# Kernel optimization log

Hardware: AMD Instinct MI355X
Metric: run time of the kernel (lower is better)

The kernel has to match this reference:

```python
import jax, jax.numpy as jnp
import numpy as np

WINDOW = (7, 7, 7)
DIM = 192
HEADS = 6
B_ = 256
NW = 32
N = int(np.prod(WINDOW))


def _relative_position_index(window_size):
    coords = np.stack(np.meshgrid(*[np.arange(w) for w in window_size], indexing='ij'))
    cf = coords.reshape(len(window_size), -1)  # (3, N)
    rel = cf[:, :, None] - cf[:, None, :]      # (3, N, N)
    rel = rel.transpose(1, 2, 0).copy()        # (N, N, 3)
    for i, w in enumerate(window_size):
        rel[:, :, i] += w - 1
    rel[:, :, 0] *= (2 * window_size[1] - 1) * (2 * window_size[2] - 1)
    rel[:, :, 1] *= 2 * window_size[2] - 1
    return rel.sum(-1).astype(np.int32)       # (N, N)


def setup_inputs() -> dict:
    key = jax.random.key(0)
    ks = jax.random.split(key, 8)
    table_rows = int(np.prod([2 * w - 1 for w in WINDOW]))  # 2197
    s = 0.02
    return {
        'skip': jax.random.normal(ks[0], (B_, N, DIM), jnp.float32),
        'x_up': jax.random.normal(ks[1], (B_, N, DIM), jnp.float32),
        'mask': jax.random.normal(ks[2], (NW, N, N), jnp.float32),
        'rel_index': jnp.asarray(_relative_position_index(WINDOW)),
        'table': s * jax.random.normal(ks[3], (table_rows, HEADS), jnp.float32),
        'kv_w': jax.random.normal(ks[4], (DIM, 2 * DIM), jnp.float32) / np.sqrt(DIM),
        'kv_b': jnp.zeros((2 * DIM,), jnp.float32),
        'proj_w': jax.random.normal(ks[5], (DIM, DIM), jnp.float32) / np.sqrt(DIM),
        'proj_b': jnp.zeros((DIM,), jnp.float32),
    }


def reference(skip, x_up, mask, rel_index, table, kv_w, kv_b, proj_w, proj_b):
    B, n, C = skip.shape
    H = HEADS
    D = C // H
    scale = D ** -0.5
    # kv projection: (B, N, 2C) -> k, v each (B, H, N, D)
    kv = skip @ kv_w + kv_b
    kv = kv.reshape(B, n, 2, H, D)
    k = kv[:, :, 0].transpose(0, 2, 1, 3)
    v = kv[:, :, 1].transpose(0, 2, 1, 3)
    q = (x_up.reshape(B, n, H, D).transpose(0, 2, 1, 3)) * scale
    attn = jnp.einsum('bhnd,bhmd->bhnm', q, k)  # (B, H, N, N)
    # gathered relative position bias: (N, N, H) -> (H, N, N)
    bias = table[rel_index].transpose(2, 0, 1)
    attn = attn + bias[None]
    nW = mask.shape[0]
    attn = attn.reshape(B // nW, nW, H, n, n) + mask[None, :, None]
    attn = jax.nn.softmax(attn.reshape(B, H, n, n), axis=-1)
    x = jnp.einsum('bhnm,bhmd->bhnd', attn, v)
    x = x.transpose(0, 2, 1, 3).reshape(B, n, C)
    return x @ proj_w + proj_b
```

## Files before the change

kernel.cpp:

```cpp
#include <hip/hip_runtime.h>
#include <hip/hip_bf16.h>

#define B_  256
#define N_  343
#define C_  192
#define H_  6
#define D_  32
#define NW_ 32
#define NN_ (N_*N_)
#define TROWS 2197
#define NP_ 352
#define PLANE (NP_*NP_)

typedef unsigned int  uint32;
typedef unsigned short u16;
typedef __attribute__((ext_vector_type(8))) short bf16x8;
typedef __attribute__((ext_vector_type(4))) float f32x4;

union frag8 { uint4 u4; bf16x8 h8; short s[8]; };

__device__ __forceinline__ float bf2f(u16 u){
  union { uint32 u; float f; } v; v.u = ((uint32)u) << 16; return v.f;
}
__device__ __forceinline__ u16 f2bf(float f){
  union { float f; uint32 u; } v; v.f = f;
  uint32 u = v.u;
  return (u16)((u + 0x7FFFu + ((u >> 16) & 1u)) >> 16);
}

__device__ __forceinline__ bool detect_f32(const uint32* w){
  int c = 0;
  #pragma unroll
  for (int u = 0; u < 32; u++){
    int e = (w[u*37] >> 7) & 0xFF;
    c += (e > 150);
  }
  return c >= 3;
}
__device__ __forceinline__ float ldf(const void* p, size_t i, bool f32){
  return f32 ? ((const float*)p)[i] : bf2f(((const u16*)p)[i]);
}
__device__ __forceinline__ void stf(void* p, size_t i, float v, bool f32){
  if (f32) ((float*)p)[i] = v;
  else     ((u16*)p)[i]   = f2bf(v);
}

__device__ __forceinline__ int klsidx(int j, int d){
  return j*32 + ((((d>>3) ^ ((j>>2)&3)))<<3) + (d&7);
}
__device__ __forceinline__ int vtidx(int d, int j){
  return d*352 + ((((j>>3) ^ ((d>>2)&3)))<<3) + (j&7);
}

__device__ __forceinline__ uint4 ld_row8(const void* __restrict__ src, bool F32,
                                         int b, int grow, int col){
  if (grow >= N_) return make_uint4(0,0,0,0);
  size_t g = ((size_t)b*N_ + grow)*C_ + col;
  if (F32){
    const float* gp = (const float*)src + g;
    float4 f0 = *(const float4*)gp, f1 = *(const float4*)(gp + 4);
    frag8 fv;
    fv.s[0]=(short)f2bf(f0.x); fv.s[1]=(short)f2bf(f0.y);
    fv.s[2]=(short)f2bf(f0.z); fv.s[3]=(short)f2bf(f0.w);
    fv.s[4]=(short)f2bf(f1.x); fv.s[5]=(short)f2bf(f1.y);
    fv.s[6]=(short)f2bf(f1.z); fv.s[7]=(short)f2bf(f1.w);
    return fv.u4;
  }
  return *(const uint4*)((const u16*)src + g);
}


__global__ void prep_bp(const void* __restrict__ skip, const int* __restrict__ rel,
                        const void* __restrict__ table, u16* __restrict__ bp){
  const bool F32 = detect_f32((const uint32*)skip);
  size_t gid = ((size_t)blockIdx.x*256 + threadIdx.x)*8;
  int p   = (int)(gid / PLANE);
  int rem = (int)(gid % PLANE);
  int i = rem / NP_, j0 = rem % NP_;
  frag8 o;
  #pragma unroll
  for (int m = 0; m < 8; m++){
    int j = j0 + m; float v = 0.f;
    if (i < N_ && j < N_){
      int r = rel[i*N_ + j];
      v = ldf(table, (size_t)r*H_ + p, F32);
    }
    o.s[m] = (short)f2bf(v);
  }
  *(uint4*)&bp[gid] = o.u4;
}

__global__ void prep_bm2(const void* __restrict__ skip, const void* __restrict__ mask,
                         const u16* __restrict__ bp, u16* __restrict__ bm){
  const bool F32 = detect_f32((const uint32*)skip);
  const float LOG2E = 1.4426950408889634f;
  size_t gid = ((size_t)blockIdx.x*256 + threadIdx.x)*8;
  int pl  = (int)(gid / PLANE);
  int rem = (int)(gid % PLANE);
  int i = rem / NP_, j0 = rem % NP_;
  int w = pl / H_, h = pl % H_;
  frag8 bg; bg.u4 = *(const uint4*)&bp[(size_t)h*PLANE + rem];
  frag8 o;
  #pragma unroll
  for (int m = 0; m < 8; m++){
    int j = j0 + m;
    float v = bf2f((u16)bg.s[m]);
    if (i < N_ && j < N_) v += ldf(mask, (size_t)w*NN_ + (size_t)i*N_ + j, F32);
    o.s[m] = (short)f2bf(v * LOG2E);
  }
  *(uint4*)&bm[gid] = o.u4;
}

__global__ __launch_bounds__(512, 2) void kv_gemm5(
    const void* __restrict__ skip, const void* __restrict__ kv_w,
    const void* __restrict__ kv_b, u16* __restrict__ kvws){
  __shared__ __align__(16) u16 sk[32*200];
  const bool F32 = detect_f32((const uint32*)skip);
  const int b = blockIdx.x;
  const int t = threadIdx.x, lane = t & 63, wave = t >> 6;
  const int n16 = lane & 15, q = lane >> 4;

  float kvb[3];
  u16*  p3[3];
  int   d3[3], isK[3];
  frag8 bw[3][6];
  #pragma unroll
  for (int c3 = 0; c3 < 3; c3++){
    int col = (wave*3 + c3)*16 + n16;
    kvb[c3] = ldf(kv_b, col, F32);
    #pragma unroll
    for (int ks = 0; ks < 6; ks++)
      #pragma unroll
      for (int j = 0; j < 8; j++)
        bw[c3][ks].s[j] = (short)f2bf(ldf(kv_w, (size_t)(ks*32 + q*8 + j)*384 + col, F32));
    if (col < 192){
      int h = col >> 5; d3[c3] = col & 31; isK[c3] = 1;
      p3[c3] = kvws + (size_t)(b*H_ + h)*22528;
    } else {
      int cv = col - 192; int h = cv >> 5; d3[c3] = cv & 31; isK[c3] = 0;
      p3[c3] = kvws + (size_t)(b*H_ + h)*22528 + 11264;
    }
  }

  const int r0 = t/24,        c0 = (t%24)*8;
  const int r1 = (t+512)/24,  c1 = ((t+512)%24)*8;
  const bool two = (t < 256);
  uint4 pre0 = ld_row8(skip, F32, b, r0, c0);
  uint4 pre1 = two ? ld_row8(skip, F32, b, r1, c1) : make_uint4(0,0,0,0);

  for (int rc = 0; rc < 11; rc++){
    __syncthreads();
    *(uint4*)&sk[r0*200 + c0] = pre0;
    if (two) *(uint4*)&sk[r1*200 + c1] = pre1;
    __syncthreads();
    if (rc < 10){
      int rb = (rc+1)*32;
      pre0 = ld_row8(skip, F32, b, rb + r0, c0);
      if (two) pre1 = ld_row8(skip, F32, b, rb + r1, c1);
    }
    frag8 af[2][6];
    #pragma unroll
    for (int half = 0; half < 2; half++)
      #pragma unroll
      for (int ks = 0; ks < 6; ks++)
        af[half][ks].u4 = *(const uint4*)&sk[(half*16 + n16)*200 + ks*32 + q*8];
    #pragma unroll
    for (int c3 = 0; c3 < 3; c3++){
      #pragma unroll
      for (int half = 0; half < 2; half++){
        f32x4 acc = {0.f,0.f,0.f,0.f};
        #pragma unroll
        for (int ks = 0; ks < 6; ks++)
          acc = __builtin_amdgcn_mfma_f32_16x16x32_bf16(af[half][ks].h8, bw[c3][ks].h8, acc, 0,0,0);
        #pragma unroll
        for (int r = 0; r < 4; r++){
          int grow = rc*32 + half*16 + q*4 + r;
          u16 val = f2bf(acc[r] + kvb[c3]);
          if (isK[c3]) p3[c3][klsidx(grow, d3[c3])] = val;
          else         p3[c3][vtidx(d3[c3], grow)] = val;
        }
      }
    }
  }
}

#define A2_VT  11264
#define A2_TOT 22528

__global__ __launch_bounds__(512, 6) void attn2(
    const void* __restrict__ skip, const void* __restrict__ x_up,
    const u16* __restrict__ bm, const u16* __restrict__ kvws,
    u16* __restrict__ xws, void* __restrict__ out){
  __shared__ __align__(16) u16 sm[A2_TOT];
  const bool F32 = detect_f32((const uint32*)skip);
  const int bid = blockIdx.x;
  const int b = bid / H_, h = bid % H_;
  const int w = b & (NW_-1);
  const int t = threadIdx.x, lane = t & 63, wave = t >> 6;
  const int n16 = lane & 15, q = lane >> 4;

  {
    const uint4* src = (const uint4*)(kvws + (size_t)bid*22528);
    uint4* dst = (uint4*)sm;
    for (int u = t; u < 2816; u += 512) dst[u] = src[u];
  }
  __syncthreads();

  const u16* bmp = bm + (size_t)(w*H_ + h)*PLANE;
  const float SC2 = 0.17677669529663687f * 1.4426950408889634f;

  for (int it = wave; it < 22; it += 8){
    int i0 = it*16;
    const u16* bmr = bmp + (size_t)(i0 + n16)*NP_;
    frag8 aq;
    {
      int qrow = min(i0 + n16, N_-1);
      size_t base = ((size_t)b*N_ + qrow)*C_ + h*D_ + q*8;
      if (F32){
        const float* xf = (const float*)x_up + base;
        float4 f0 = *(const float4*)xf, f1 = *(const float4*)(xf + 4);
        aq.s[0]=(short)f2bf(f0.x); aq.s[1]=(short)f2bf(f0.y);
        aq.s[2]=(short)f2bf(f0.z); aq.s[3]=(short)f2bf(f0.w);
        aq.s[4]=(short)f2bf(f1.x); aq.s[5]=(short)f2bf(f1.y);
        aq.s[6]=(short)f2bf(f1.z); aq.s[7]=(short)f2bf(f1.w);
      } else {
        aq.u4 = *(const uint4*)((const u16*)x_up + base);
      }
    }
    f32x4 O0 = {0.f,0.f,0.f,0.f}, O1 = {0.f,0.f,0.f,0.f};
    float lp = 0.f;
    for (int jc = 0; jc < 11; jc++){
      int j0 = jc*32;
      uint2 mba = *(const uint2*)&bmr[j0 + q*4];
      uint2 mbb = *(const uint2*)&bmr[j0 + 16 + q*4];
      frag8 bk0, bk1;
      bk0.u4 = *(const uint4*)&sm[klsidx(j0 + n16, q*8)];
      bk1.u4 = *(const uint4*)&sm[klsidx(j0 + 16 + n16, q*8)];
      f32x4 z = {0.f,0.f,0.f,0.f};
      f32x4 s0 = __builtin_amdgcn_mfma_f32_16x16x32_bf16(bk0.h8, aq.h8, z, 0,0,0);
      f32x4 s1 = __builtin_amdgcn_mfma_f32_16x16x32_bf16(bk1.h8, aq.h8, z, 0,0,0);
      union { uint2 v; u16 e[4]; } Ua, Ub;
      Ua.v = mba; Ub.v = mbb;
      float pa[4], pb[4];
      #pragma unroll
      for (int r = 0; r < 4; r++){
        pa[r] = exp2f(fmaf(s0[r], SC2, bf2f(Ua.e[r])));
        float eb = exp2f(fmaf(s1[r], SC2, bf2f(Ub.e[r])));
        pb[r] = (j0 + 16 + q*4 + r < N_) ? eb : 0.f;
        lp += pa[r] + pb[r];
      }
      uint32 A0, A1, B0, B1;
      asm("v_cvt_pk_bf16_f32 %0, %1, %2" : "=v"(A0) : "v"(pa[0]), "v"(pa[1]));
      asm("v_cvt_pk_bf16_f32 %0, %1, %2" : "=v"(A1) : "v"(pa[2]), "v"(pa[3]));
      asm("v_cvt_pk_bf16_f32 %0, %1, %2" : "=v"(B0) : "v"(pb[0]), "v"(pb[1]));
      asm("v_cvt_pk_bf16_f32 %0, %1, %2" : "=v"(B1) : "v"(pb[2]), "v"(pb[3]));
      int src0 = ((q & 1) << 5) + n16;
      int src1 = src0 + 16;
      uint32 a0s = (uint32)__shfl((int)A0, src0), a1s = (uint32)__shfl((int)A1, src0);
      uint32 a2s = (uint32)__shfl((int)A0, src1), a3s = (uint32)__shfl((int)A1, src1);
      uint32 b0s = (uint32)__shfl((int)B0, src0), b1s = (uint32)__shfl((int)B1, src0);
      uint32 b2s = (uint32)__shfl((int)B0, src1), b3s = (uint32)__shfl((int)B1, src1);
      bool lo = (q < 2);
      frag8 ap;
      ap.u4.x = lo ? a0s : b0s;
      ap.u4.y = lo ? a1s : b1s;
      ap.u4.z = lo ? a2s : b2s;
      ap.u4.w = lo ? a3s : b3s;
      frag8 bv0, bv1;
      bv0.u4 = *(const uint4*)&sm[A2_VT + vtidx(n16,      j0 + q*8)];
      bv1.u4 = *(const uint4*)&sm[A2_VT + vtidx(16 + n16, j0 + q*8)];
      O0 = __builtin_amdgcn_mfma_f32_16x16x32_bf16(ap.h8, bv0.h8, O0, 0,0,0);
      O1 = __builtin_amdgcn_mfma_f32_16x16x32_bf16(ap.h8, bv1.h8, O1, 0,0,0);
    }
    lp += __shfl_xor(lp, 16);
    lp += __shfl_xor(lp, 32);
    #pragma unroll
    for (int r = 0; r < 4; r++){
      int il = q*4 + r;
      float rl = 1.f / __shfl(lp, (lane & 48) | il);
      int i = i0 + il;
      if (i < N_){
        if (xws){
          u16* xp = xws + ((size_t)(b*H_ + h)*N_ + i)*D_;
          xp[n16]      = f2bf(O0[r]*rl);
          xp[16 + n16] = f2bf(O1[r]*rl);
        } else {
          size_t ob = ((size_t)b*N_ + i)*C_ + h*D_;
          stf(out, ob + n16,      O0[r]*rl, F32);
          stf(out, ob + 16 + n16, O1[r]*rl, F32);
        }
      }
    }
  }
}

__global__ __launch_bounds__(256, 4) void proj3(const u16* __restrict__ xws,
                                                void* __restrict__ outp,
                                                const void* __restrict__ pw,
                                                const void* __restrict__ pb,
                                                const void* __restrict__ skip){
  __shared__ __align__(16) u16 xs[64*200];
  const bool F32 = detect_f32((const uint32*)skip);
  const int t = threadIdx.x, lane = t & 63, wave = t >> 6;
  const int n16 = lane & 15, q = lane >> 4;
  const size_t row0 = (size_t)blockIdx.x * 64;

  for (int u = t; u < 1536; u += 256){
    int r = u / 24, c8 = u % 24;
    int g = (int)row0 + r;
    int b = g / N_, i = g - b*N_;
    int h = c8 >> 2, d0 = (c8 & 3)*8;
    uint4 vv = *(const uint4*)&xws[((size_t)(b*H_ + h)*N_ + i)*D_ + d0];
    *(uint4*)&xs[r*200 + h*32 + d0] = vv;
  }
  frag8 bwf[3][6];
  float pbv[3];
  #pragma unroll
  for (int c3 = 0; c3 < 3; c3++){
    int col = (wave*3 + c3)*16 + n16;
    pbv[c3] = ldf(pb, col, F32);
    #pragma unroll
    for (int ks = 0; ks < 6; ks++)
      #pragma unroll
      for (int j = 0; j < 8; j++)
        bwf[c3][ks].s[j] = (short)f2bf(ldf(pw, (size_t)(ks*32 + q*8 + j)*C_ + col, F32));
  }
  __syncthreads();
  for (int rt = 0; rt < 4; rt++){
    frag8 af[6];
    #pragma unroll
    for (int ks = 0; ks < 6; ks++)
      af[ks].u4 = *(const uint4*)&xs[(rt*16 + n16)*200 + ks*32 + q*8];
    #pragma unroll
    for (int c3 = 0; c3 < 3; c3++){
      f32x4 acc = {0.f,0.f,0.f,0.f};
      #pragma unroll
      for (int ks = 0; ks < 6; ks++)
        acc = __builtin_amdgcn_mfma_f32_16x16x32_bf16(af[ks].h8, bwf[c3][ks].h8, acc, 0,0,0);
      int col = (wave*3 + c3)*16 + n16;
      #pragma unroll
      for (int r = 0; r < 4; r++)
        stf(outp, (row0 + rt*16 + q*4 + r)*C_ + col, acc[r] + pbv[c3], F32);
    }
  }
}


__global__ void prep_biasg(const void* __restrict__ skip, const int* __restrict__ rel,
                           const void* __restrict__ table, u16* __restrict__ biasg){
  const bool F32 = detect_f32((const uint32*)skip);
  int idx = blockIdx.x*256 + threadIdx.x;
  if (idx >= NN_) return;
  int r = rel[idx];
  #pragma unroll
  for (int h = 0; h < H_; h++)
    biasg[(size_t)h*NN_ + idx] = f2bf(ldf(table, (size_t)r*H_ + h, F32));
}

#define KLS_OFF 6400
#define VT_OFF  (KLS_OFF + 352*40)
#define SMEM_U16 (VT_OFF + 32*360)

__global__ __launch_bounds__(512, 4) void attn_fused(
    const void* __restrict__ skip, const void* __restrict__ x_up,
    const void* __restrict__ mask, const u16* __restrict__ biasg,
    const void* __restrict__ kv_w, const void* __restrict__ kv_b,
    void* __restrict__ out){
  __shared__ __align__(16) u16 sm[SMEM_U16];
  const bool F32 = detect_f32((const uint32*)skip);
  const int bid = blockIdx.x;
  const int b = bid / H_, h = bid % H_;
  const int w = b & (NW_-1);
  const int t = threadIdx.x;
  const int lane = t & 63, wave = t >> 6;
  const int n16 = lane & 15, q = lane >> 4;
  const int colt = wave & 3;
  const int half = wave >> 2;
  const int gcol = (colt < 2) ? (h*D_ + colt*16 + n16)
                              : (C_ + h*D_ + (colt-2)*16 + n16);
  const float kvb = ldf(kv_b, gcol, F32);
  frag8 bw[6];
  #pragma unroll
  for (int ks = 0; ks < 6; ks++)
    #pragma unroll
    for (int j = 0; j < 8; j++)
      bw[ks].s[j] = (short)f2bf(ldf(kv_w, (size_t)(ks*32 + q*8 + j)*384 + gcol, F32));

  for (int rc = 0; rc < 11; rc++){
    __syncthreads();
    for (int u = t; u < 32*C_; u += 512){
      int r = u / C_, c = u % C_;
      int grow = rc*32 + r;
      float v = (grow < N_) ? ldf(skip, ((size_t)b*N_ + grow)*C_ + c, F32) : 0.f;
      sm[r*200 + c] = f2bf(v);
    }
    __syncthreads();
    f32x4 acc = {0.f, 0.f, 0.f, 0.f};
    #pragma unroll
    for (int ks = 0; ks < 6; ks++){
      frag8 a;  a.u4 = *(const uint4*)&sm[(half*16 + n16)*200 + ks*32 + q*8];
      acc = __builtin_amdgcn_mfma_f32_16x16x32_bf16(a.h8, bw[ks].h8, acc, 0, 0, 0);
    }
    #pragma unroll
    for (int r = 0; r < 4; r++){
      int grow = rc*32 + half*16 + q*4 + r;
      u16 val = f2bf(acc[r] + kvb);
      if (colt < 2) sm[KLS_OFF + grow*40 + colt*16 + n16] = val;
      else          sm[VT_OFF + ((colt-2)*16 + n16)*360 + grow] = val;
    }
  }
  __syncthreads();

  const float scale = 0.17677669529663687f;
  const size_t mwb = (size_t)w*NN_;
  const u16* bg = biasg + (size_t)h*NN_;
  u16* pls = &sm[wave*640];
  for (int it = wave; it < 22; it += 8){
    int i0 = it*16;
    {
      int rrow = min(i0 + (lane >> 2), N_-1);
      int col0 = (lane & 3)*8;
      size_t gb = ((size_t)b*N_ + rrow)*C_ + h*D_ + col0;
      u16* dst = &pls[(lane >> 2)*40 + col0];
      #pragma unroll
      for (int m = 0; m < 8; m++) dst[m] = f2bf(ldf(x_up, gb + m, F32) * scale);
    }
    frag8 aq; aq.u4 = *(const uint4*)&pls[n16*40 + q*8];
    f32x4 O0 = {0.f,0.f,0.f,0.f}, O1 = {0.f,0.f,0.f,0.f};
    float lp[4] = {0.f, 0.f, 0.f, 0.f};
    int ic[4];
    #pragma unroll
    for (int r = 0; r < 4; r++) ic[r] = min(i0 + q*4 + r, N_-1);
    for (int jc = 0; jc < 11; jc++){
      int j0 = jc*32;
      int ja = j0 + n16, jb = j0 + 16 + n16;
      int jac = min(ja, N_-1), jbc = min(jb, N_-1);
      float bma[4], bmb[4];
      #pragma unroll
      for (int r = 0; r < 4; r++){
        size_t rb = (size_t)ic[r]*N_;
        bma[r] = bf2f(bg[rb + jac]) + ldf(mask, mwb + rb + jac, F32);
        bmb[r] = bf2f(bg[rb + jbc]) + ldf(mask, mwb + rb + jbc, F32);
      }
      frag8 bk0, bk1;
      bk0.u4 = *(const uint4*)&sm[KLS_OFF + (j0 + n16)*40 + q*8];
      bk1.u4 = *(const uint4*)&sm[KLS_OFF + (j0 + 16 + n16)*40 + q*8];
      f32x4 z = {0.f,0.f,0.f,0.f};
      f32x4 s0 = __builtin_amdgcn_mfma_f32_16x16x32_bf16(aq.h8, bk0.h8, z, 0,0,0);
      f32x4 s1 = __builtin_amdgcn_mfma_f32_16x16x32_bf16(aq.h8, bk1.h8, z, 0,0,0);
      #pragma unroll
      for (int r = 0; r < 4; r++){
        float pa = (ja < N_) ? __expf(s0[r] + bma[r] - 12.f) : 0.f;
        float pb = (jb < N_) ? __expf(s1[r] + bmb[r] - 12.f) : 0.f;
        lp[r] += pa + pb;
        pls[(q*4 + r)*40 + n16]      = f2bf(pa);
        pls[(q*4 + r)*40 + 16 + n16] = f2bf(pb);
      }
      frag8 ap; ap.u4 = *(const uint4*)&pls[n16*40 + q*8];
      frag8 bv0, bv1;
      bv0.u4 = *(const uint4*)&sm[VT_OFF + n16*360 + j0 + q*8];
      bv1.u4 = *(const uint4*)&sm[VT_OFF + (16 + n16)*360 + j0 + q*8];
      O0 = __builtin_amdgcn_mfma_f32_16x16x32_bf16(ap.h8, bv0.h8, O0, 0,0,0);
      O1 = __builtin_amdgcn_mfma_f32_16x16x32_bf16(ap.h8, bv1.h8, O1, 0,0,0);
    }
    #pragma unroll
    for (int msk = 1; msk < 16; msk <<= 1){
      #pragma unroll
      for (int r = 0; r < 4; r++) lp[r] += __shfl_xor(lp[r], msk, 64);
    }
    #pragma unroll
    for (int r = 0; r < 4; r++){
      int i = i0 + q*4 + r;
      if (i < N_){
        float rl = 1.f / lp[r];
        size_t ob = ((size_t)b*N_ + i)*C_ + h*D_;
        stf(out, ob + n16,      O0[r]*rl, F32);
        stf(out, ob + 16 + n16, O1[r]*rl, F32);
      }
    }
  }
}

__global__ __launch_bounds__(256, 6) void proj2(void* __restrict__ io,
                                                const void* __restrict__ pw,
                                                const void* __restrict__ pb,
                                                const void* __restrict__ skip){
  __shared__ __align__(16) u16 xs[64*200];
  const bool F32 = detect_f32((const uint32*)skip);
  const int t = threadIdx.x;
  const int lane = t & 63, wave = t >> 6;
  const int n16 = lane & 15, q = lane >> 4;
  const size_t row0 = (size_t)blockIdx.x * 64;

  for (int u = t; u < 64*C_/8; u += 256){
    int r = u / 24, c = (u % 24)*8;
    size_t g = (row0 + r)*C_ + c;
    uint4 vv;
    if (F32){
      const float* gp = (const float*)io + g;
      float4 f0 = *(const float4*)gp, f1 = *(const float4*)(gp + 4);
      frag8 fv;
      fv.s[0]=(short)f2bf(f0.x); fv.s[1]=(short)f2bf(f0.y);
      fv.s[2]=(short)f2bf(f0.z); fv.s[3]=(short)f2bf(f0.w);
      fv.s[4]=(short)f2bf(f1.x); fv.s[5]=(short)f2bf(f1.y);
      fv.s[6]=(short)f2bf(f1.z); fv.s[7]=(short)f2bf(f1.w);
      vv = fv.u4;
    } else {
      vv = *(const uint4*)((const u16*)io + g);
    }
    *(uint4*)&xs[r*200 + c] = vv;
  }
  __syncthreads();
  for (int c3 = 0; c3 < 3; c3++){
    int col = (wave*3 + c3)*16 + n16;
    float pbv = ldf(pb, col, F32);
    frag8 bwf[6];
    #pragma unroll
    for (int ks = 0; ks < 6; ks++)
      #pragma unroll
      for (int j = 0; j < 8; j++)
        bwf[ks].s[j] = (short)f2bf(ldf(pw, (size_t)(ks*32 + q*8 + j)*C_ + col, F32));
    for (int rt = 0; rt < 4; rt++){
      frag8 af[6];
      #pragma unroll
      for (int ks = 0; ks < 6; ks++)
        af[ks].u4 = *(const uint4*)&xs[(rt*16 + n16)*200 + ks*32 + q*8];
      f32x4 acc = {0.f,0.f,0.f,0.f};
      #pragma unroll
      for (int ks = 0; ks < 6; ks++)
        acc = __builtin_amdgcn_mfma_f32_16x16x32_bf16(af[ks].h8, bwf[ks].h8, acc, 0,0,0);
      #pragma unroll
      for (int r = 0; r < 4; r++)
        stf(io, (row0 + rt*16 + q*4 + r)*C_ + col, acc[r] + pbv, F32);
    }
  }
}

extern "C" void kernel_launch(void* const* d_in, const int* in_sizes, int n_in,
                              void* d_out, int out_size, void* d_ws, size_t ws_size,
                              hipStream_t stream){
  (void)in_sizes; (void)n_in; (void)out_size;
  const void* skip  = d_in[0];
  const void* x_up  = d_in[1];
  const void* mask  = d_in[2];
  const int*  rel   = (const int*)d_in[3];
  const void* table = d_in[4];
  const void* kv_w  = d_in[5];
  const void* kv_b  = d_in[6];
  const void* pw    = d_in[7];
  const void* pb    = d_in[8];

  const size_t BM_BYTES = (size_t)192*PLANE*2;
  const size_t KV_BYTES = (size_t)B_*H_*45056;
  const size_t BP_BYTES = (size_t)H_*PLANE*2;
  const size_t XW_BYTES = (size_t)B_*H_*N_*D_*2;

  if (ws_size >= BM_BYTES + KV_BYTES + XW_BYTES){
    u16* bm   = (u16*)d_ws;
    u16* kvws = (u16*)((char*)d_ws + BM_BYTES);
    u16* xws  = (u16*)((char*)d_ws + BM_BYTES + KV_BYTES);
    u16* bp   = xws;
    prep_bp <<<(H_*PLANE/8)/256, 256, 0, stream>>>(skip, rel, table, bp);
    prep_bm2<<<(192*PLANE/8)/256, 256, 0, stream>>>(skip, mask, bp, bm);
    kv_gemm5<<<B_, 512, 0, stream>>>(skip, kv_w, kv_b, kvws);
    attn2   <<<B_*H_, 512, 0, stream>>>(skip, x_up, bm, kvws, xws, d_out);
    proj3   <<<87808/64, 256, 0, stream>>>(xws, d_out, pw, pb, skip);
  } else if (ws_size >= BM_BYTES + KV_BYTES + BP_BYTES){
    u16* bm   = (u16*)d_ws;
    u16* kvws = (u16*)((char*)d_ws + BM_BYTES);
    u16* bp   = (u16*)((char*)d_ws + BM_BYTES + KV_BYTES);
    prep_bp <<<(H_*PLANE/8)/256, 256, 0, stream>>>(skip, rel, table, bp);
    prep_bm2<<<(192*PLANE/8)/256, 256, 0, stream>>>(skip, mask, bp, bm);
    kv_gemm5<<<B_, 512, 0, stream>>>(skip, kv_w, kv_b, kvws);
    attn2   <<<B_*H_, 512, 0, stream>>>(skip, x_up, bm, kvws, nullptr, d_out);
    proj2   <<<87808/64, 256, 0, stream>>>(d_out, pw, pb, skip);
  } else {
    u16* biasg = (u16*)d_ws;
    prep_biasg<<<(NN_+255)/256, 256, 0, stream>>>(skip, rel, table, biasg);
    attn_fused<<<B_*H_, 512, 0, stream>>>(skip, x_up, mask, biasg, kv_w, kv_b, d_out);
    proj2     <<<87808/64, 256, 0, stream>>>(d_out, pw, pb, skip);
  }
}
```

Measured before the change: 449.6 us.

## Double-buffer kv GEMM smem tiles, specialize attention tail masking, raise proj occupancy

The kv projection kernel now uses two shared-memory tiles, so the next row chunk is written to the alternate buffer while the current one is consumed. This drops one of the two barriers per iteration. The attention kernel hoists shuffle indices out of the loop and applies the column bound check only on the last key chunk, removing per-element comparisons elsewhere. The projection kernel's launch bound occupancy hint rises from 4 to 6 blocks, which may force register spills.

After: 560.1 us. 1.25x slower.

```diff
diff --git a/kernel.cpp b/kernel.cpp
--- a/kernel.cpp
+++ b/kernel.cpp
@@ -111,10 +111,10 @@
   *(uint4*)&bm[gid] = o.u4;
 }
 
-__global__ __launch_bounds__(512, 2) void kv_gemm5(
+__global__ __launch_bounds__(512, 2) void kv_gemm6(
     const void* __restrict__ skip, const void* __restrict__ kv_w,
     const void* __restrict__ kv_b, u16* __restrict__ kvws){
-  __shared__ __align__(16) u16 sk[32*200];
+  __shared__ __align__(16) u16 sk[2][32*200];
   const bool F32 = detect_f32((const uint32*)skip);
   const int b = blockIdx.x;
   const int t = threadIdx.x, lane = t & 63, wave = t >> 6;
@@ -145,25 +145,35 @@
   const int r0 = t/24,        c0 = (t%24)*8;
   const int r1 = (t+512)/24,  c1 = ((t+512)%24)*8;
   const bool two = (t < 256);
-  uint4 pre0 = ld_row8(skip, F32, b, r0, c0);
-  uint4 pre1 = two ? ld_row8(skip, F32, b, r1, c1) : make_uint4(0,0,0,0);
+
+  {
+    uint4 a0 = ld_row8(skip, F32, b, r0, c0);
+    uint4 a1 = two ? ld_row8(skip, F32, b, r1, c1) : make_uint4(0,0,0,0);
+    *(uint4*)&sk[0][r0*200 + c0] = a0;
+    if (two) *(uint4*)&sk[0][r1*200 + c1] = a1;
+  }
+  uint4 cur0 = ld_row8(skip, F32, b, 32 + r0, c0);
+  uint4 cur1 = two ? ld_row8(skip, F32, b, 32 + r1, c1) : make_uint4(0,0,0,0);
+  __syncthreads();
 
   for (int rc = 0; rc < 11; rc++){
-    __syncthreads();
-    *(uint4*)&sk[r0*200 + c0] = pre0;
-    if (two) *(uint4*)&sk[r1*200 + c1] = pre1;
-    __syncthreads();
+    const u16* buf = sk[rc & 1];
+    frag8 af[2][6];
+    #pragma unroll
+    for (int half = 0; half < 2; half++)
+      #pragma unroll
+      for (int ks = 0; ks < 6; ks++)
+        af[half][ks].u4 = *(const uint4*)&buf[(half*16 + n16)*200 + ks*32 + q*8];
     if (rc < 10){
-      int rb = (rc+1)*32;
-      pre0 = ld_row8(skip, F32, b, rb + r0, c0);
-      if (two) pre1 = ld_row8(skip, F32, b, rb + r1, c1);
-    }
-    frag8 af[2][6];
-    #pragma unroll
-    for (int half = 0; half < 2; half++)
-      #pragma unroll
-      for (int ks = 0; ks < 6; ks++)
-        af[half][ks].u4 = *(const uint4*)&sk[(half*16 + n16)*200 + ks*32 + q*8];
+      u16* nbuf = sk[(rc + 1) & 1];
+      *(uint4*)&nbuf[r0*200 + c0] = cur0;
+      if (two) *(uint4*)&nbuf[r1*200 + c1] = cur1;
+      if (rc < 9){
+        int rb = (rc + 2)*32;
+        cur0 = ld_row8(skip, F32, b, rb + r0, c0);
+        if (two) cur1 = ld_row8(skip, F32, b, rb + r1, c1);
+      }
+    }
     #pragma unroll
     for (int c3 = 0; c3 < 3; c3++){
       #pragma unroll
@@ -181,6 +191,7 @@
         }
       }
     }
+    __syncthreads();
   }
 }
 
@@ -208,6 +219,9 @@
 
   const u16* bmp = bm + (size_t)(w*H_ + h)*PLANE;
   const float SC2 = 0.17677669529663687f * 1.4426950408889634f;
+  const int src0 = ((q & 1) << 5) + n16;
+  const int src1 = src0 + 16;
+  const bool lo = (q < 2);
 
   for (int it = wave; it < 22; it += 8){
     int i0 = it*16;
@@ -242,25 +256,31 @@
       union { uint2 v; u16 e[4]; } Ua, Ub;
       Ua.v = mba; Ub.v = mbb;
       float pa[4], pb[4];
-      #pragma unroll
-      for (int r = 0; r < 4; r++){
-        pa[r] = exp2f(fmaf(s0[r], SC2, bf2f(Ua.e[r])));
-        float eb = exp2f(fmaf(s1[r], SC2, bf2f(Ub.e[r])));
-        pb[r] = (j0 + 16 + q*4 + r < N_) ? eb : 0.f;
-        lp += pa[r] + pb[r];
+      if (jc < 10){
+        #pragma unroll
+        for (int r = 0; r < 4; r++){
+          pa[r] = exp2f(fmaf(s0[r], SC2, bf2f(Ua.e[r])));
+          pb[r] = exp2f(fmaf(s1[r], SC2, bf2f(Ub.e[r])));
+          lp += pa[r] + pb[r];
+        }
+      } else {
+        #pragma unroll
+        for (int r = 0; r < 4; r++){
+          pa[r] = exp2f(fmaf(s0[r], SC2, bf2f(Ua.e[r])));
+          float eb = exp2f(fmaf(s1[r], SC2, bf2f(Ub.e[r])));
+          pb[r] = (336 + q*4 + r < N_) ? eb : 0.f;
+          lp += pa[r] + pb[r];
+        }
       }
       uint32 A0, A1, B0, B1;
       asm("v_cvt_pk_bf16_f32 %0, %1, %2" : "=v"(A0) : "v"(pa[0]), "v"(pa[1]));
       asm("v_cvt_pk_bf16_f32 %0, %1, %2" : "=v"(A1) : "v"(pa[2]), "v"(pa[3]));
       asm("v_cvt_pk_bf16_f32 %0, %1, %2" : "=v"(B0) : "v"(pb[0]), "v"(pb[1]));
       asm("v_cvt_pk_bf16_f32 %0, %1, %2" : "=v"(B1) : "v"(pb[2]), "v"(pb[3]));
-      int src0 = ((q & 1) << 5) + n16;
-      int src1 = src0 + 16;
       uint32 a0s = (uint32)__shfl((int)A0, src0), a1s = (uint32)__shfl((int)A1, src0);
       uint32 a2s = (uint32)__shfl((int)A0, src1), a3s = (uint32)__shfl((int)A1, src1);
       uint32 b0s = (uint32)__shfl((int)B0, src0), b1s = (uint32)__shfl((int)B1, src0);
       uint32 b2s = (uint32)__shfl((int)B0, src1), b3s = (uint32)__shfl((int)B1, src1);
-      bool lo = (q < 2);
       frag8 ap;
       ap.u4.x = lo ? a0s : b0s;
       ap.u4.y = lo ? a1s : b1s;
@@ -294,7 +314,7 @@
   }
 }
 
-__global__ __launch_bounds__(256, 4) void proj3(const u16* __restrict__ xws,
+__global__ __launch_bounds__(256, 6) void proj3(const u16* __restrict__ xws,
                                                 void* __restrict__ outp,
                                                 const void* __restrict__ pw,
                                                 const void* __restrict__ pb,
@@ -562,7 +582,7 @@
     u16* bp   = xws;
     prep_bp <<<(H_*PLANE/8)/256, 256, 0, stream>>>(skip, rel, table, bp);
     prep_bm2<<<(192*PLANE/8)/256, 256, 0, stream>>>(skip, mask, bp, bm);
-    kv_gemm5<<<B_, 512, 0, stream>>>(skip, kv_w, kv_b, kvws);
+    kv_gemm6<<<B_, 512, 0, stream>>>(skip, kv_w, kv_b, kvws);
     attn2   <<<B_*H_, 512, 0, stream>>>(skip, x_up, bm, kvws, xws, d_out);
     proj3   <<<87808/64, 256, 0, stream>>>(xws, d_out, pw, pb, skip);
   } else if (ws_size >= BM_BYTES + KV_BYTES + BP_BYTES){
@@ -571,7 +591,7 @@
     u16* bp   = (u16*)((char*)d_ws + BM_BYTES + KV_BYTES);
     prep_bp <<<(H_*PLANE/8)/256, 256, 0, stream>>>(skip, rel, table, bp);
     prep_bm2<<<(192*PLANE/8)/256, 256, 0, stream>>>(skip, mask, bp, bm);
-    kv_gemm5<<<B_, 512, 0, stream>>>(skip, kv_w, kv_b, kvws);
+    kv_gemm6<<<B_, 512, 0, stream>>>(skip, kv_w, kv_b, kvws);
     attn2   <<<B_*H_, 512, 0, stream>>>(skip, x_up, bm, kvws, nullptr, d_out);
     proj2   <<<87808/64, 256, 0, stream>>>(d_out, pw, pb, skip);
   } else {
```
